# Kernel tuning notes

Hardware: AMD Instinct MI355X
Metric: run time of the kernel (lower is better)

Reference implementation:

```python
import jax, jax.numpy as jnp
import numpy as np

D_MODEL = 256
NS = 8


def _linear_params(key, out_f, in_f):
    s = 1.0 / np.sqrt(in_f)
    kw, kb = jax.random.split(key)
    W = jax.random.uniform(kw, (out_f, in_f), jnp.float32, -s, s)
    b = jax.random.uniform(kb, (out_f,), jnp.float32, -s, s)
    return W, b


def setup_inputs() -> dict:
    key = jax.random.key(0)
    ks = jax.random.split(key, 8)
    B, NQ = 2, 10000
    C, D, H, W = D_MODEL, 16, 64, 64
    Wdp, bdp = _linear_params(ks[3], NS * 3, D_MODEL)
    Wa, ba = _linear_params(ks[4], NS, D_MODEL)
    Wv, bv = _linear_params(ks[5], D_MODEL, D_MODEL)
    Ww, bw = _linear_params(ks[6], D_MODEL, D_MODEL)
    Wo, bo = _linear_params(ks[7], D_MODEL, D_MODEL)
    return {
        "query": jax.random.normal(ks[0], (B, NQ, D_MODEL), jnp.float32),
        "ref_points": jax.random.uniform(ks[1], (B, NQ, 3), jnp.float32, -1.0, 1.0),
        "image_features": jax.random.normal(ks[2], (B, C, D, H, W), jnp.float32),
        "mask": jnp.ones((B, 2, NQ), dtype=bool),
        "Wdp": Wdp, "bdp": bdp,
        "Wa": Wa, "ba": ba,
        "Wv": Wv, "bv": bv,
        "Ww": Ww, "bw": bw,
        "Wo": Wo, "bo": bo,
    }


def grid_sample_3d(vol, grid):
    """Trilinear grid_sample, align_corners=True, zero padding.
    vol: (B,C,D,H,W); grid: (B,N,P,3) with (x,y,z) in [-1,1] (x indexes W).
    Returns (B,N,P,C)."""
    B, C, D, H, W = vol.shape
    vol_t = jnp.transpose(vol, (0, 2, 3, 4, 1))  # (B,D,H,W,C)
    ix = (grid[..., 0] + 1.0) * 0.5 * (W - 1)
    iy = (grid[..., 1] + 1.0) * 0.5 * (H - 1)
    iz = (grid[..., 2] + 1.0) * 0.5 * (D - 1)
    x0 = jnp.floor(ix); y0 = jnp.floor(iy); z0 = jnp.floor(iz)
    fx = ix - x0; fy = iy - y0; fz = iz - z0

    def gather(v, zi, yi, xi):  # v: (D,H,W,C); indices (N,P)
        return v[zi, yi, xi]  # (N,P,C)

    out = jnp.zeros(grid.shape[:-1] + (C,), vol.dtype)
    for dz in (0, 1):
        for dy in (0, 1):
            for dx in (0, 1):
                xi = x0 + dx; yi = y0 + dy; zi = z0 + dz
                w = ((fx if dx else 1.0 - fx)
                     * (fy if dy else 1.0 - fy)
                     * (fz if dz else 1.0 - fz))
                valid = ((xi >= 0) & (xi <= W - 1)
                         & (yi >= 0) & (yi <= H - 1)
                         & (zi >= 0) & (zi <= D - 1))
                xc = jnp.clip(xi, 0, W - 1).astype(jnp.int32)
                yc = jnp.clip(yi, 0, H - 1).astype(jnp.int32)
                zc = jnp.clip(zi, 0, D - 1).astype(jnp.int32)
                vals = jax.vmap(gather)(vol_t, zc, yc, xc)  # (B,N,P,C)
                out = out + (w * valid)[..., None] * vals
    return out


def reference(query, ref_points, image_features, mask,
              Wdp, bdp, Wa, ba, Wv, bv, Ww, bw, Wo, bo):
    B, NQ, C = query.shape
    n_points = NS
    # learned offsets around reference points
    delta_p = (query @ Wdp.T + bdp).reshape(B, NQ, n_points, 3)
    p_delta_p = ref_points[:, :, None, :] + delta_p
    # reorder dims [1,0,2] -> grid (x,y,z) convention of grid_sample
    grid = p_delta_p[..., jnp.array([1, 0, 2])]
    sampled = grid_sample_3d(image_features, grid)  # (B,NQ,Ns,C)
    v = sampled @ Wv.T + bv          # value_proj
    wv = v @ Ww.T + bw               # W
    attn = jax.nn.softmax(query @ Wa.T + ba, axis=-1)  # (B,NQ,Ns)
    summed = jnp.einsum('bnpc,bnp->bnc', wv, attn)
    m = jnp.any(mask, axis=1)  # (B,NQ)
    summed = summed * m[..., None]
    return summed @ Wo.T + bo
```

## Files before the change

### kernel.cpp

```cpp
#include <hip/hip_runtime.h>

#define NQ    10000
#define BATCH 2
#define CDIM  256
#define DD    16
#define HH    64
#define WW    64

using bf16x8 = __attribute__((ext_vector_type(8))) short;
using f32x4  = __attribute__((ext_vector_type(4))) float;

__device__ __forceinline__ unsigned short f2bf(float f) {
    unsigned int u = __float_as_uint(f);
    u = u + 0x7FFFu + ((u >> 16) & 1u);
    return (unsigned short)(u >> 16);
}
__device__ __forceinline__ float bf2f(unsigned short h) {
    return __uint_as_float(((unsigned int)h) << 16);
}

__global__ __launch_bounds__(256) void k_transpose_bf16(const float* __restrict__ vol,
                                                        unsigned short* __restrict__ volt) {
    __shared__ float tile[64][65];
    int bid  = blockIdx.x;
    int cblk = bid & 3;
    int y    = (bid >> 2) & 63;
    int z    = (bid >> 8) & 15;
    int b    = bid >> 12;
    int tid  = threadIdx.x;
    int lx   = tid & 63, wy = tid >> 6;

    const float* src = vol + (size_t)(b * CDIM + cblk * 64) * (DD * HH * WW)
                           + (size_t)z * (HH * WW) + y * WW;
#pragma unroll
    for (int i = 0; i < 16; ++i) {
        int cl = wy * 16 + i;
        tile[cl][lx] = src[(size_t)cl * (DD * HH * WW) + lx];
    }
    __syncthreads();
    unsigned int* dst32 = reinterpret_cast<unsigned int*>(
        volt + ((size_t)(b * DD + z) * HH + y) * WW * CDIM) + cblk * 32;
    int cp = tid & 31;
#pragma unroll
    for (int i = 0; i < 8; ++i) {
        int x = i * 8 + (tid >> 5);
        unsigned int uo = (unsigned int)f2bf(tile[cp * 2][x])
                        | ((unsigned int)f2bf(tile[cp * 2 + 1][x]) << 16);
        dst32[(size_t)x * (CDIM / 2) + cp] = uo;
    }
}

template <bool BF16OUT>
__global__ __launch_bounds__(256) void k_combine(const float* __restrict__ A,
                                                 const float* __restrict__ B,
                                                 const float* __restrict__ bin,
                                                 const float* __restrict__ badd,
                                                 void* __restrict__ outW,
                                                 float* __restrict__ outb) {
    int i = blockIdx.x, j = threadIdx.x;
    __shared__ __align__(16) float row[256];
    __shared__ float red[4];
    row[j] = A[i * 256 + j];
    __syncthreads();
    float a0 = 0.f, a1 = 0.f, a2 = 0.f, a3 = 0.f;
#pragma unroll 4
    for (int k = 0; k < 256; k += 4) {
        a0 = fmaf(row[k + 0], B[(k + 0) * 256 + j], a0);
        a1 = fmaf(row[k + 1], B[(k + 1) * 256 + j], a1);
        a2 = fmaf(row[k + 2], B[(k + 2) * 256 + j], a2);
        a3 = fmaf(row[k + 3], B[(k + 3) * 256 + j], a3);
    }
    float acc = (a0 + a1) + (a2 + a3);
    if (BF16OUT)
        ((unsigned short*)outW)[i * 256 + j] = f2bf(acc);
    else
        ((float*)outW)[i * 256 + j] = acc;

    float pb = row[j] * bin[j];
    for (int off = 32; off; off >>= 1) pb += __shfl_down(pb, off, 64);
    int lane = j & 63, wv_ = j >> 6;
    if (lane == 0) red[wv_] = pb;
    __syncthreads();
    if (j == 0) outb[i] = red[0] + red[1] + red[2] + red[3] + badd[i];
}

__device__ __forceinline__ void geom_issue(
    int p, const float* __restrict__ dotsw, const float* __restrict__ bdp,
    float r0, float r1, float r2, float a,
    const ushort4* __restrict__ vb4, int lane,
    ushort4 (&u)[8], float (&wt)[8]) {
    float ix = fmaf(r1 + dotsw[p * 3 + 1] + bdp[p * 3 + 1], 31.5f, 31.5f);
    float iy = fmaf(r0 + dotsw[p * 3 + 0] + bdp[p * 3 + 0], 31.5f, 31.5f);
    float iz = fmaf(r2 + dotsw[p * 3 + 2] + bdp[p * 3 + 2], 7.5f, 7.5f);
    float xf = floorf(ix), yf = floorf(iy), zf = floorf(iz);
    float fx = ix - xf, fy = iy - yf, fz = iz - zf;
    int x0 = (int)xf, y0 = (int)yf, z0 = (int)zf;
    int xc[2], yc[2], zc[2];
    float wx[2], wy2[2], wz2[2];
#pragma unroll
    for (int d = 0; d < 2; ++d) {
        int xi = x0 + d, yi = y0 + d, zi = z0 + d;
        wx[d]  = (xi >= 0 && xi < WW) ? (d ? fx : 1.f - fx) : 0.f;
        wy2[d] = (yi >= 0 && yi < HH) ? (d ? fy : 1.f - fy) : 0.f;
        wz2[d] = ((zi >= 0 && zi < DD) ? (d ? fz : 1.f - fz) : 0.f) * a;
        xc[d] = min(max(xi, 0), WW - 1);
        yc[d] = min(max(yi, 0), HH - 1);
        zc[d] = min(max(zi, 0), DD - 1);
    }
    float wzy[4];
#pragma unroll
    for (int zz = 0; zz < 2; ++zz)
#pragma unroll
        for (int yy = 0; yy < 2; ++yy) wzy[zz * 2 + yy] = wz2[zz] * wy2[yy];
#pragma unroll
    for (int c = 0; c < 8; ++c) {
        int dz = c >> 2, dy = (c >> 1) & 1, dx = c & 1;
        wt[c] = wzy[dz * 2 + dy] * wx[dx];
        int off = (zc[dz] * HH + yc[dy]) * WW + xc[dx];
        off = __builtin_amdgcn_readfirstlane(off);
        u[c] = vb4[(size_t)off * (CDIM / 4) + lane];
    }
}

__device__ __forceinline__ void proc8(const ushort4 (&u)[8], const float (&wt)[8],
                                      float4& acc) {
#pragma unroll
    for (int c = 0; c < 8; ++c) {
        acc.x = fmaf(wt[c], bf2f(u[c].x), acc.x);
        acc.y = fmaf(wt[c], bf2f(u[c].y), acc.y);
        acc.z = fmaf(wt[c], bf2f(u[c].z), acc.z);
        acc.w = fmaf(wt[c], bf2f(u[c].w), acc.w);
    }
}

template <bool USE_VOLT>
__global__ __launch_bounds__(256) void k_sample4(
    const float* __restrict__ query, const float* __restrict__ refp,
    const float* __restrict__ vol, const unsigned short* __restrict__ voltb,
    const float* __restrict__ Wdp, const float* __restrict__ bdp,
    const float* __restrict__ Wa, const float* __restrict__ ba,
    unsigned short* __restrict__ S) {
    int tid = threadIdx.x, w = tid >> 6, lane = tid & 63;
    int g = lane >> 4, ch = lane & 15;
    int bq0 = blockIdx.x * 4;
    __shared__ float dots[4][32];

    {
        float4 qv[4][4];
#pragma unroll
        for (int q = 0; q < 4; ++q)
#pragma unroll
            for (int i = 0; i < 4; ++i)
                qv[q][i] = *reinterpret_cast<const float4*>(
                    query + (size_t)(bq0 + q) * 256 + ch * 16 + i * 4);
#pragma unroll
        for (int rr = 0; rr < 2; ++rr) {
            int row = w * 8 + rr * 4 + g;
            const float* rp = (row < 24) ? (Wdp + row * 256) : (Wa + (row - 24) * 256);
            float4 wv4[4];
#pragma unroll
            for (int i = 0; i < 4; ++i)
                wv4[i] = *reinterpret_cast<const float4*>(rp + ch * 16 + i * 4);
#pragma unroll
            for (int q = 0; q < 4; ++q) {
                float s = 0.f;
#pragma unroll
                for (int i = 0; i < 4; ++i)
                    s = fmaf(wv4[i].x, qv[q][i].x, fmaf(wv4[i].y, qv[q][i].y,
                        fmaf(wv4[i].z, qv[q][i].z, fmaf(wv4[i].w, qv[q][i].w, s))));
                s += __shfl_xor(s, 1); s += __shfl_xor(s, 2);
                s += __shfl_xor(s, 4); s += __shfl_xor(s, 8);
                if (ch == q) dots[q][row] = s;
            }
        }
    }
    __syncthreads();

    int bq = bq0 + w, b = bq / NQ;
    const float* dotsw = dots[w];
    float lg[8]; float mx = -1e30f;
#pragma unroll
    for (int p = 0; p < 8; ++p) { lg[p] = dotsw[24 + p] + ba[p]; mx = fmaxf(mx, lg[p]); }
    float se = 0.f;
#pragma unroll
    for (int p = 0; p < 8; ++p) { lg[p] = __expf(lg[p] - mx); se += lg[p]; }
    float inv = 1.f / se;
    float r0 = refp[bq * 3 + 0], r1 = refp[bq * 3 + 1], r2 = refp[bq * 3 + 2];

    float4 acc = make_float4(0.f, 0.f, 0.f, 0.f);
    if (USE_VOLT) {
        const ushort4* vb4 = reinterpret_cast<const ushort4*>(
            voltb + (size_t)b * (DD * HH * WW) * CDIM);
        ushort4 u0[8], u1[8];
        float w0a[8], w1a[8];
        geom_issue(0, dotsw, bdp, r0, r1, r2, lg[0] * inv, vb4, lane, u0, w0a);
#pragma unroll
        for (int p = 0; p < 7; ++p) {
            if ((p & 1) == 0) {
                geom_issue(p + 1, dotsw, bdp, r0, r1, r2, lg[p + 1] * inv, vb4, lane, u1, w1a);
                proc8(u0, w0a, acc);
            } else {
                geom_issue(p + 1, dotsw, bdp, r0, r1, r2, lg[p + 1] * inv, vb4, lane, u0, w0a);
                proc8(u1, w1a, acc);
            }
        }
        proc8(u1, w1a, acc);
    } else {
        const float* vf = vol + (size_t)b * CDIM * (DD * HH * WW);
#pragma unroll
        for (int p = 0; p < 8; ++p) {
            ushort4 ud[8]; float wtd[8];
            float a = lg[p] * inv;
            float ix = fmaf(r1 + dotsw[p * 3 + 1] + bdp[p * 3 + 1], 31.5f, 31.5f);
            float iy = fmaf(r0 + dotsw[p * 3 + 0] + bdp[p * 3 + 0], 31.5f, 31.5f);
            float iz = fmaf(r2 + dotsw[p * 3 + 2] + bdp[p * 3 + 2], 7.5f, 7.5f);
            float xf = floorf(ix), yf = floorf(iy), zf = floorf(iz);
            float fx = ix - xf, fy = iy - yf, fz = iz - zf;
            int x0 = (int)xf, y0 = (int)yf, z0 = (int)zf;
            int xc[2], yc[2], zc[2]; float wx[2], wy2[2], wz2[2];
#pragma unroll
            for (int d = 0; d < 2; ++d) {
                int xi = x0 + d, yi = y0 + d, zi = z0 + d;
                wx[d]  = (xi >= 0 && xi < WW) ? (d ? fx : 1.f - fx) : 0.f;
                wy2[d] = (yi >= 0 && yi < HH) ? (d ? fy : 1.f - fy) : 0.f;
                wz2[d] = ((zi >= 0 && zi < DD) ? (d ? fz : 1.f - fz) : 0.f) * a;
                xc[d] = min(max(xi, 0), WW - 1);
                yc[d] = min(max(yi, 0), HH - 1);
                zc[d] = min(max(zi, 0), DD - 1);
            }
#pragma unroll
            for (int c = 0; c < 8; ++c) {
                int dz = c >> 2, dy = (c >> 1) & 1, dx = c & 1;
                float wgt = wz2[dz] * wy2[dy] * wx[dx];
                int off = (zc[dz] * HH + yc[dy]) * WW + xc[dx];
#pragma unroll
                for (int cc = 0; cc < 4; ++cc) {
                    float v = vf[(size_t)(lane * 4 + cc) * (DD * HH * WW) + off];
                    (&acc.x)[cc] = fmaf(wgt, v, (&acc.x)[cc]);
                }
            }
        }
    }
    ushort4 o;
    o.x = f2bf(acc.x); o.y = f2bf(acc.y); o.z = f2bf(acc.z); o.w = f2bf(acc.w);
    reinterpret_cast<ushort4*>(S + (size_t)bq * 256)[lane] = o;
}

__global__ __launch_bounds__(256) void k_gemm_mx(
    const unsigned short* __restrict__ A,
    const unsigned short* __restrict__ Bw,
    const float* __restrict__ bias,
    const float* __restrict__ bo,
    const int* __restrict__ mask,
    float* __restrict__ C, int M) {
    const int LDT = 40;
    __shared__ unsigned short As[64 * LDT];
    __shared__ unsigned short Bs[64 * LDT];
    int tid = threadIdx.x, wv = tid >> 6, lane = tid & 63;
    int row0 = blockIdx.x * 64, col0 = blockIdx.y * 64;
    int wr = (wv & 1) * 32, wc = (wv >> 1) * 32;
    f32x4 acc[2][2] = {};

    int sr = tid >> 2, skc = tid & 3;
    for (int k0 = 0; k0 < 256; k0 += 32) {
        int gr = row0 + sr;
        uint4 av = make_uint4(0u, 0u, 0u, 0u);
        if (gr < M)
            av = *reinterpret_cast<const uint4*>(A + (size_t)gr * 256 + k0 + skc * 8);
        *reinterpret_cast<uint4*>(&As[sr * LDT + skc * 8]) = av;
        uint4 bv = *reinterpret_cast<const uint4*>(Bw + (size_t)(col0 + sr) * 256 + k0 + skc * 8);
        *reinterpret_cast<uint4*>(&Bs[sr * LDT + skc * 8]) = bv;
        __syncthreads();
        bf16x8 af[2], bf[2];
#pragma unroll
        for (int mi = 0; mi < 2; ++mi)
            af[mi] = *reinterpret_cast<const bf16x8*>(
                &As[(wr + mi * 16 + (lane & 15)) * LDT + (lane >> 4) * 8]);
#pragma unroll
        for (int ni = 0; ni < 2; ++ni)
            bf[ni] = *reinterpret_cast<const bf16x8*>(
                &Bs[(wc + ni * 16 + (lane & 15)) * LDT + (lane >> 4) * 8]);
#pragma unroll
        for (int mi = 0; mi < 2; ++mi)
#pragma unroll
            for (int ni = 0; ni < 2; ++ni)
                acc[mi][ni] = __builtin_amdgcn_mfma_f32_16x16x32_bf16(
                    af[mi], bf[ni], acc[mi][ni], 0, 0, 0);
        __syncthreads();
    }

    int lc = lane & 15, lr4 = (lane >> 4) * 4;
    float biasv[2], bov[2];
#pragma unroll
    for (int ni = 0; ni < 2; ++ni) {
        int col = col0 + wc + ni * 16 + lc;
        biasv[ni] = bias[col];
        bov[ni]   = bo[col];
    }
#pragma unroll
    for (int mi = 0; mi < 2; ++mi)
#pragma unroll
        for (int r = 0; r < 4; ++r) {
            int row = row0 + wr + mi * 16 + lr4 + r;
            if (row >= M) continue;
            int b = row / NQ, q = row - b * NQ;
            bool mv = (mask[(b * 2 + 0) * NQ + q] | mask[(b * 2 + 1) * NQ + q]) != 0;
#pragma unroll
            for (int ni = 0; ni < 2; ++ni) {
                int col = col0 + wc + ni * 16 + lc;
                C[(size_t)row * 256 + col] = mv ? (acc[mi][ni][r] + biasv[ni]) : bov[ni];
            }
        }
}

extern "C" void kernel_launch(void* const* d_in, const int* in_sizes, int n_in,
                              void* d_out, int out_size, void* d_ws, size_t ws_size,
                              hipStream_t stream) {
    const float* query = (const float*)d_in[0];
    const float* refp  = (const float*)d_in[1];
    const float* vol   = (const float*)d_in[2];
    const int*   mask  = (const int*)d_in[3];
    const float* Wdp   = (const float*)d_in[4];
    const float* bdp   = (const float*)d_in[5];
    const float* Wa    = (const float*)d_in[6];
    const float* ba    = (const float*)d_in[7];
    const float* Wv    = (const float*)d_in[8];
    const float* bv    = (const float*)d_in[9];
    const float* Ww    = (const float*)d_in[10];
    const float* bw    = (const float*)d_in[11];
    const float* Wo    = (const float*)d_in[12];
    const float* bo    = (const float*)d_in[13];
    float* out = (float*)d_out;

    char* ws = (char*)d_ws;
    const size_t M = (size_t)BATCH * NQ;
    size_t o_S    = 0;
    size_t o_W12  = o_S + M * 256 * 2;
    size_t o_b12  = o_W12 + 256 * 256 * 4;
    size_t o_W123 = o_b12 + 1024;
    size_t o_b123 = o_W123 + 256 * 256 * 2;
    size_t o_volt = (o_b123 + 1024 + 255) & ~(size_t)255;
    size_t need_volt = o_volt + (size_t)BATCH * DD * HH * WW * CDIM * 2;
    bool use_volt = ws_size >= need_volt;

    unsigned short* Sb   = (unsigned short*)(ws + o_S);
    float*          W12  = (float*)(ws + o_W12);
    float*          b12  = (float*)(ws + o_b12);
    unsigned short* W123 = (unsigned short*)(ws + o_W123);
    float*          b123 = (float*)(ws + o_b123);
    unsigned short* volt = (unsigned short*)(ws + o_volt);

    if (use_volt)
        k_transpose_bf16<<<BATCH * DD * HH * (CDIM / 64), 256, 0, stream>>>(vol, volt);
    k_combine<false><<<256, 256, 0, stream>>>(Ww, Wv, bv, bw, W12, b12);
    k_combine<true ><<<256, 256, 0, stream>>>(Wo, W12, b12, bo, W123, b123);

    if (use_volt)
        k_sample4<true><<<(int)(M / 4), 256, 0, stream>>>(query, refp, vol, volt,
                                                          Wdp, bdp, Wa, ba, Sb);
    else
        k_sample4<false><<<(int)(M / 4), 256, 0, stream>>>(query, refp, vol, volt,
                                                           Wdp, bdp, Wa, ba, Sb);

    dim3 g((unsigned)((M + 63) / 64), 4);
    k_gemm_mx<<<g, 256, 0, stream>>>(Sb, W123, b123, bo, mask, out, (int)M);
}
```

Baseline: 135.8 us.

## Split offset/attention projection into separate kernel, slim sampling kernel

Moves the query projection for sampling offsets and attention logits out of the sampling kernel into a new k_dots kernel. That kernel writes 32 biased dot products per query to workspace, and each wave handles 4 queries over all 32 rows. The sampling kernel now only loads those 32 floats, drops shared memory and __syncthreads, and takes launch bounds of (256,4) for higher occupancy. BF16 unpacking now uses uint2 with shift and mask instead of ushort4 conversions. The cost is an extra kernel launch plus a round trip of the dot products through global memory.

Result: slower. 145.8 us (+7.4%).

```diff
diff --git a/kernel.cpp b/kernel.cpp
--- a/kernel.cpp
+++ b/kernel.cpp
@@ -14,9 +14,6 @@
     unsigned int u = __float_as_uint(f);
     u = u + 0x7FFFu + ((u >> 16) & 1u);
     return (unsigned short)(u >> 16);
-}
-__device__ __forceinline__ float bf2f(unsigned short h) {
-    return __uint_as_float(((unsigned int)h) << 16);
 }
 
 __global__ __launch_bounds__(256) void k_transpose_bf16(const float* __restrict__ vol,
@@ -84,140 +81,91 @@
     if (j == 0) outb[i] = red[0] + red[1] + red[2] + red[3] + badd[i];
 }
 
-__device__ __forceinline__ void geom_issue(
-    int p, const float* __restrict__ dotsw, const float* __restrict__ bdp,
-    float r0, float r1, float r2, float a,
-    const ushort4* __restrict__ vb4, int lane,
-    ushort4 (&u)[8], float (&wt)[8]) {
-    float ix = fmaf(r1 + dotsw[p * 3 + 1] + bdp[p * 3 + 1], 31.5f, 31.5f);
-    float iy = fmaf(r0 + dotsw[p * 3 + 0] + bdp[p * 3 + 0], 31.5f, 31.5f);
-    float iz = fmaf(r2 + dotsw[p * 3 + 2] + bdp[p * 3 + 2], 7.5f, 7.5f);
-    float xf = floorf(ix), yf = floorf(iy), zf = floorf(iz);
-    float fx = ix - xf, fy = iy - yf, fz = iz - zf;
-    int x0 = (int)xf, y0 = (int)yf, z0 = (int)zf;
-    int xc[2], yc[2], zc[2];
-    float wx[2], wy2[2], wz2[2];
-#pragma unroll
-    for (int d = 0; d < 2; ++d) {
-        int xi = x0 + d, yi = y0 + d, zi = z0 + d;
-        wx[d]  = (xi >= 0 && xi < WW) ? (d ? fx : 1.f - fx) : 0.f;
-        wy2[d] = (yi >= 0 && yi < HH) ? (d ? fy : 1.f - fy) : 0.f;
-        wz2[d] = ((zi >= 0 && zi < DD) ? (d ? fz : 1.f - fz) : 0.f) * a;
-        xc[d] = min(max(xi, 0), WW - 1);
-        yc[d] = min(max(yi, 0), HH - 1);
-        zc[d] = min(max(zi, 0), DD - 1);
-    }
-    float wzy[4];
-#pragma unroll
-    for (int zz = 0; zz < 2; ++zz)
-#pragma unroll
-        for (int yy = 0; yy < 2; ++yy) wzy[zz * 2 + yy] = wz2[zz] * wy2[yy];
-#pragma unroll
-    for (int c = 0; c < 8; ++c) {
-        int dz = c >> 2, dy = (c >> 1) & 1, dx = c & 1;
-        wt[c] = wzy[dz * 2 + dy] * wx[dx];
-        int off = (zc[dz] * HH + yc[dy]) * WW + xc[dx];
-        off = __builtin_amdgcn_readfirstlane(off);
-        u[c] = vb4[(size_t)off * (CDIM / 4) + lane];
-    }
-}
-
-__device__ __forceinline__ void proc8(const ushort4 (&u)[8], const float (&wt)[8],
-                                      float4& acc) {
-#pragma unroll
-    for (int c = 0; c < 8; ++c) {
-        acc.x = fmaf(wt[c], bf2f(u[c].x), acc.x);
-        acc.y = fmaf(wt[c], bf2f(u[c].y), acc.y);
-        acc.z = fmaf(wt[c], bf2f(u[c].z), acc.z);
-        acc.w = fmaf(wt[c], bf2f(u[c].w), acc.w);
-    }
-}
-
-template <bool USE_VOLT>
-__global__ __launch_bounds__(256) void k_sample4(
-    const float* __restrict__ query, const float* __restrict__ refp,
-    const float* __restrict__ vol, const unsigned short* __restrict__ voltb,
+__global__ __launch_bounds__(256) void k_dots(
+    const float* __restrict__ query,
     const float* __restrict__ Wdp, const float* __restrict__ bdp,
     const float* __restrict__ Wa, const float* __restrict__ ba,
+    float* __restrict__ dotsG) {
+    int tid = threadIdx.x, w = tid >> 6, lane = tid & 63;
+    int g = lane >> 4, ch = lane & 15;
+    int bq0 = blockIdx.x * 16 + w * 4;
+
+    float4 qv[4][4];
+#pragma unroll
+    for (int q = 0; q < 4; ++q)
+#pragma unroll
+        for (int i = 0; i < 4; ++i)
+            qv[q][i] = *reinterpret_cast<const float4*>(
+                query + (size_t)(bq0 + q) * 256 + ch * 16 + i * 4);
+
+#pragma unroll
+    for (int rr = 0; rr < 8; ++rr) {
+        int rowi = rr * 4 + g;
+        const float* rp = (rowi < 24) ? (Wdp + rowi * 256) : (Wa + (rowi - 24) * 256);
+        float bia = (rowi < 24) ? bdp[rowi] : ba[rowi - 24];
+        float4 wv4[4];
+#pragma unroll
+        for (int i = 0; i < 4; ++i)
+            wv4[i] = *reinterpret_cast<const float4*>(rp + ch * 16 + i * 4);
+#pragma unroll
+        for (int q = 0; q < 4; ++q) {
+            float s = 0.f;
+#pragma unroll
+            for (int i = 0; i < 4; ++i)
+                s = fmaf(wv4[i].x, qv[q][i].x, fmaf(wv4[i].y, qv[q][i].y,
+                    fmaf(wv4[i].z, qv[q][i].z, fmaf(wv4[i].w, qv[q][i].w, s))));
+            s += __shfl_xor(s, 1); s += __shfl_xor(s, 2);
+            s += __shfl_xor(s, 4); s += __shfl_xor(s, 8);
+            if (ch == q) dotsG[(size_t)(bq0 + q) * 32 + rowi] = s + bia;
+        }
+    }
+}
+
+template <bool USE_VOLT>
+__global__ __launch_bounds__(256, 4) void k_sample5(
+    const float* __restrict__ refp,
+    const float* __restrict__ vol,
+    const unsigned short* __restrict__ voltb,
+    const float* __restrict__ dotsG,
     unsigned short* __restrict__ S) {
     int tid = threadIdx.x, w = tid >> 6, lane = tid & 63;
-    int g = lane >> 4, ch = lane & 15;
-    int bq0 = blockIdx.x * 4;
-    __shared__ float dots[4][32];
-
+    int bq = blockIdx.x * 4 + w, b = bq / NQ;
+
+    float dt[32];
     {
-        float4 qv[4][4];
-#pragma unroll
-        for (int q = 0; q < 4; ++q)
-#pragma unroll
-            for (int i = 0; i < 4; ++i)
-                qv[q][i] = *reinterpret_cast<const float4*>(
-                    query + (size_t)(bq0 + q) * 256 + ch * 16 + i * 4);
-#pragma unroll
-        for (int rr = 0; rr < 2; ++rr) {
-            int row = w * 8 + rr * 4 + g;
-            const float* rp = (row < 24) ? (Wdp + row * 256) : (Wa + (row - 24) * 256);
-            float4 wv4[4];
-#pragma unroll
-            for (int i = 0; i < 4; ++i)
-                wv4[i] = *reinterpret_cast<const float4*>(rp + ch * 16 + i * 4);
-#pragma unroll
-            for (int q = 0; q < 4; ++q) {
-                float s = 0.f;
-#pragma unroll
-                for (int i = 0; i < 4; ++i)
-                    s = fmaf(wv4[i].x, qv[q][i].x, fmaf(wv4[i].y, qv[q][i].y,
-                        fmaf(wv4[i].z, qv[q][i].z, fmaf(wv4[i].w, qv[q][i].w, s))));
-                s += __shfl_xor(s, 1); s += __shfl_xor(s, 2);
-                s += __shfl_xor(s, 4); s += __shfl_xor(s, 8);
-                if (ch == q) dots[q][row] = s;
-            }
-        }
-    }
-    __syncthreads();
-
-    int bq = bq0 + w, b = bq / NQ;
-    const float* dotsw = dots[w];
+        const float4* dr = reinterpret_cast<const float4*>(dotsG + (size_t)bq * 32);
+#pragma unroll
+        for (int j = 0; j < 8; ++j) {
+            float4 t = dr[j];
+            dt[4 * j + 0] = t.x; dt[4 * j + 1] = t.y;
+            dt[4 * j + 2] = t.z; dt[4 * j + 3] = t.w;
+        }
+    }
     float lg[8]; float mx = -1e30f;
 #pragma unroll
-    for (int p = 0; p < 8; ++p) { lg[p] = dotsw[24 + p] + ba[p]; mx = fmaxf(mx, lg[p]); }
+    for (int p = 0; p < 8; ++p) { lg[p] = dt[24 + p]; mx = fmaxf(mx, lg[p]); }
     float se = 0.f;
 #pragma unroll
     for (int p = 0; p < 8; ++p) { lg[p] = __expf(lg[p] - mx); se += lg[p]; }
     float inv = 1.f / se;
     float r0 = refp[bq * 3 + 0], r1 = refp[bq * 3 + 1], r2 = refp[bq * 3 + 2];
 
-    float4 acc = make_float4(0.f, 0.f, 0.f, 0.f);
+    float a0 = 0.f, a1 = 0.f, a2 = 0.f, a3 = 0.f;
+
     if (USE_VOLT) {
-        const ushort4* vb4 = reinterpret_cast<const ushort4*>(
+        const uint2* vb = reinterpret_cast<const uint2*>(
             voltb + (size_t)b * (DD * HH * WW) * CDIM);
-        ushort4 u0[8], u1[8];
-        float w0a[8], w1a[8];
-        geom_issue(0, dotsw, bdp, r0, r1, r2, lg[0] * inv, vb4, lane, u0, w0a);
-#pragma unroll
-        for (int p = 0; p < 7; ++p) {
-            if ((p & 1) == 0) {
-                geom_issue(p + 1, dotsw, bdp, r0, r1, r2, lg[p + 1] * inv, vb4, lane, u1, w1a);
-                proc8(u0, w0a, acc);
-            } else {
-                geom_issue(p + 1, dotsw, bdp, r0, r1, r2, lg[p + 1] * inv, vb4, lane, u0, w0a);
-                proc8(u1, w1a, acc);
-            }
-        }
-        proc8(u1, w1a, acc);
-    } else {
-        const float* vf = vol + (size_t)b * CDIM * (DD * HH * WW);
-#pragma unroll
-        for (int p = 0; p < 8; ++p) {
-            ushort4 ud[8]; float wtd[8];
+
+        auto geom = [&](int p, uint2 (&u)[8], float (&wt)[8]) {
             float a = lg[p] * inv;
-            float ix = fmaf(r1 + dotsw[p * 3 + 1] + bdp[p * 3 + 1], 31.5f, 31.5f);
-            float iy = fmaf(r0 + dotsw[p * 3 + 0] + bdp[p * 3 + 0], 31.5f, 31.5f);
-            float iz = fmaf(r2 + dotsw[p * 3 + 2] + bdp[p * 3 + 2], 7.5f, 7.5f);
+            float ix = fmaf(r1 + dt[p * 3 + 1], 31.5f, 31.5f);
+            float iy = fmaf(r0 + dt[p * 3 + 0], 31.5f, 31.5f);
+            float iz = fmaf(r2 + dt[p * 3 + 2], 7.5f, 7.5f);
             float xf = floorf(ix), yf = floorf(iy), zf = floorf(iz);
             float fx = ix - xf, fy = iy - yf, fz = iz - zf;
             int x0 = (int)xf, y0 = (int)yf, z0 = (int)zf;
-            int xc[2], yc[2], zc[2]; float wx[2], wy2[2], wz2[2];
+            int xc[2], yc[2], zc[2];
+            float wx[2], wy2[2], wz2[2];
 #pragma unroll
             for (int d = 0; d < 2; ++d) {
                 int xi = x0 + d, yi = y0 + d, zi = z0 + d;
@@ -228,21 +176,76 @@
                 yc[d] = min(max(yi, 0), HH - 1);
                 zc[d] = min(max(zi, 0), DD - 1);
             }
+            float wzy[4];
+#pragma unroll
+            for (int zz = 0; zz < 2; ++zz)
+#pragma unroll
+                for (int yy = 0; yy < 2; ++yy) wzy[zz * 2 + yy] = wz2[zz] * wy2[yy];
+#pragma unroll
+            for (int c = 0; c < 8; ++c) {
+                int dz = c >> 2, dy = (c >> 1) & 1, dx = c & 1;
+                wt[c] = wzy[dz * 2 + dy] * wx[dx];
+                int off = (zc[dz] * HH + yc[dy]) * WW + xc[dx];
+                off = __builtin_amdgcn_readfirstlane(off);
+                u[c] = vb[(size_t)off * (CDIM / 4) + lane];
+            }
+        };
+        auto proc = [&](const uint2 (&u)[8], const float (&wt)[8]) {
+#pragma unroll
+            for (int c = 0; c < 8; ++c) {
+                float w_ = wt[c];
+                a0 = fmaf(w_, __uint_as_float(u[c].x << 16), a0);
+                a1 = fmaf(w_, __uint_as_float(u[c].x & 0xffff0000u), a1);
+                a2 = fmaf(w_, __uint_as_float(u[c].y << 16), a2);
+                a3 = fmaf(w_, __uint_as_float(u[c].y & 0xffff0000u), a3);
+            }
+        };
+
+        uint2 u0[8], u1[8];
+        float w0a[8], w1a[8];
+        geom(0, u0, w0a);
+#pragma unroll
+        for (int p = 0; p < 7; ++p) {
+            if ((p & 1) == 0) { geom(p + 1, u1, w1a); proc(u0, w0a); }
+            else              { geom(p + 1, u0, w0a); proc(u1, w1a); }
+        }
+        proc(u1, w1a);
+    } else {
+        const float* vf = vol + (size_t)b * CDIM * (DD * HH * WW);
+#pragma unroll
+        for (int p = 0; p < 8; ++p) {
+            float a = lg[p] * inv;
+            float ix = fmaf(r1 + dt[p * 3 + 1], 31.5f, 31.5f);
+            float iy = fmaf(r0 + dt[p * 3 + 0], 31.5f, 31.5f);
+            float iz = fmaf(r2 + dt[p * 3 + 2], 7.5f, 7.5f);
+            float xf = floorf(ix), yf = floorf(iy), zf = floorf(iz);
+            float fx = ix - xf, fy = iy - yf, fz = iz - zf;
+            int x0 = (int)xf, y0 = (int)yf, z0 = (int)zf;
+            int xc[2], yc[2], zc[2]; float wx[2], wy2[2], wz2[2];
+#pragma unroll
+            for (int d = 0; d < 2; ++d) {
+                int xi = x0 + d, yi = y0 + d, zi = z0 + d;
+                wx[d]  = (xi >= 0 && xi < WW) ? (d ? fx : 1.f - fx) : 0.f;
+                wy2[d] = (yi >= 0 && yi < HH) ? (d ? fy : 1.f - fy) : 0.f;
+                wz2[d] = ((zi >= 0 && zi < DD) ? (d ? fz : 1.f - fz) : 0.f) * a;
+                xc[d] = min(max(xi, 0), WW - 1);
+                yc[d] = min(max(yi, 0), HH - 1);
+                zc[d] = min(max(zi, 0), DD - 1);
+            }
 #pragma unroll
             for (int c = 0; c < 8; ++c) {
                 int dz = c >> 2, dy = (c >> 1) & 1, dx = c & 1;
                 float wgt = wz2[dz] * wy2[dy] * wx[dx];
                 int off = (zc[dz] * HH + yc[dy]) * WW + xc[dx];
-#pragma unroll
-                for (int cc = 0; cc < 4; ++cc) {
-                    float v = vf[(size_t)(lane * 4 + cc) * (DD * HH * WW) + off];
-                    (&acc.x)[cc] = fmaf(wgt, v, (&acc.x)[cc]);
-                }
+                a0 = fmaf(wgt, vf[(size_t)(lane * 4 + 0) * (DD * HH * WW) + off], a0);
+                a1 = fmaf(wgt, vf[(size_t)(lane * 4 + 1) * (DD * HH * WW) + off], a1);
+                a2 = fmaf(wgt, vf[(size_t)(lane * 4 + 2) * (DD * HH * WW) + off], a2);
+                a3 = fmaf(wgt, vf[(size_t)(lane * 4 + 3) * (DD * HH * WW) + off], a3);
             }
         }
     }
     ushort4 o;
-    o.x = f2bf(acc.x); o.y = f2bf(acc.y); o.z = f2bf(acc.z); o.w = f2bf(acc.w);
+    o.x = f2bf(a0); o.y = f2bf(a1); o.z = f2bf(a2); o.w = f2bf(a3);
     reinterpret_cast<ushort4*>(S + (size_t)bq * 256)[lane] = o;
 }
 
@@ -339,7 +342,8 @@
     size_t o_b12  = o_W12 + 256 * 256 * 4;
     size_t o_W123 = o_b12 + 1024;
     size_t o_b123 = o_W123 + 256 * 256 * 2;
-    size_t o_volt = (o_b123 + 1024 + 255) & ~(size_t)255;
+    size_t o_dots = o_b123 + 1024;
+    size_t o_volt = (o_dots + M * 32 * 4 + 255) & ~(size_t)255;
     size_t need_volt = o_volt + (size_t)BATCH * DD * HH * WW * CDIM * 2;
     bool use_volt = ws_size >= need_volt;
 
@@ -348,19 +352,19 @@
     float*          b12  = (float*)(ws + o_b12);
     unsigned short* W123 = (unsigned short*)(ws + o_W123);
     float*          b123 = (float*)(ws + o_b123);
+    float*          dots = (float*)(ws + o_dots);
     unsigned short* volt = (unsigned short*)(ws + o_volt);
 
     if (use_volt)
         k_transpose_bf16<<<BATCH * DD * HH * (CDIM / 64), 256, 0, stream>>>(vol, volt);
     k_combine<false><<<256, 256, 0, stream>>>(Ww, Wv, bv, bw, W12, b12);
     k_combine<true ><<<256, 256, 0, stream>>>(Wo, W12, b12, bo, W123, b123);
+    k_dots<<<(int)(M / 16), 256, 0, stream>>>(query, Wdp, bdp, Wa, ba, dots);
 
     if (use_volt)
-        k_sample4<true><<<(int)(M / 4), 256, 0, stream>>>(query, refp, vol, volt,
-                                                          Wdp, bdp, Wa, ba, Sb);
+        k_sample5<true><<<(int)(M / 4), 256, 0, stream>>>(refp, vol, volt, dots, Sb);
     else
-        k_sample4<false><<<(int)(M / 4), 256, 0, stream>>>(query, refp, vol, volt,
-                                                           Wdp, bdp, Wa, ba, Sb);
+        k_sample5<false><<<(int)(M / 4), 256, 0, stream>>>(refp, vol, volt, dots, Sb);
 
     dim3 g((unsigned)((M + 63) / 64), 4);
     k_gemm_mx<<<g, 256, 0, stream>>>(Sb, W123, b123, bo, mask, out, (int)M);
```

## Gather x-adjacent corner pairs with 16-byte loads split across half-waves

Applied to the files above, without the earlier changes.

The sampling kernel no longer issues 8 corner gathers of 8 bytes per lane per point. It issues 4 gathers of 16 bytes, each covering two x-adjacent voxels. Lanes 0-31 handle the left voxel and lanes 32-63 the right one, with the x weight selected per half, and a cross-half shuffle sums the partials before lanes 0-31 write 8 channels each. This halves the number of gather instructions and address computations, at the cost of a shuffle reduction and extra edge-case logic for clamped x positions.

New measurement: 213.7 us. +57.4%, slower.

```diff
diff --git a/kernel.cpp b/kernel.cpp
--- a/kernel.cpp
+++ b/kernel.cpp
@@ -14,9 +14,6 @@
     unsigned int u = __float_as_uint(f);
     u = u + 0x7FFFu + ((u >> 16) & 1u);
     return (unsigned short)(u >> 16);
-}
-__device__ __forceinline__ float bf2f(unsigned short h) {
-    return __uint_as_float(((unsigned int)h) << 16);
 }
 
 __global__ __launch_bounds__(256) void k_transpose_bf16(const float* __restrict__ vol,
@@ -84,57 +81,8 @@
     if (j == 0) outb[i] = red[0] + red[1] + red[2] + red[3] + badd[i];
 }
 
-__device__ __forceinline__ void geom_issue(
-    int p, const float* __restrict__ dotsw, const float* __restrict__ bdp,
-    float r0, float r1, float r2, float a,
-    const ushort4* __restrict__ vb4, int lane,
-    ushort4 (&u)[8], float (&wt)[8]) {
-    float ix = fmaf(r1 + dotsw[p * 3 + 1] + bdp[p * 3 + 1], 31.5f, 31.5f);
-    float iy = fmaf(r0 + dotsw[p * 3 + 0] + bdp[p * 3 + 0], 31.5f, 31.5f);
-    float iz = fmaf(r2 + dotsw[p * 3 + 2] + bdp[p * 3 + 2], 7.5f, 7.5f);
-    float xf = floorf(ix), yf = floorf(iy), zf = floorf(iz);
-    float fx = ix - xf, fy = iy - yf, fz = iz - zf;
-    int x0 = (int)xf, y0 = (int)yf, z0 = (int)zf;
-    int xc[2], yc[2], zc[2];
-    float wx[2], wy2[2], wz2[2];
-#pragma unroll
-    for (int d = 0; d < 2; ++d) {
-        int xi = x0 + d, yi = y0 + d, zi = z0 + d;
-        wx[d]  = (xi >= 0 && xi < WW) ? (d ? fx : 1.f - fx) : 0.f;
-        wy2[d] = (yi >= 0 && yi < HH) ? (d ? fy : 1.f - fy) : 0.f;
-        wz2[d] = ((zi >= 0 && zi < DD) ? (d ? fz : 1.f - fz) : 0.f) * a;
-        xc[d] = min(max(xi, 0), WW - 1);
-        yc[d] = min(max(yi, 0), HH - 1);
-        zc[d] = min(max(zi, 0), DD - 1);
-    }
-    float wzy[4];
-#pragma unroll
-    for (int zz = 0; zz < 2; ++zz)
-#pragma unroll
-        for (int yy = 0; yy < 2; ++yy) wzy[zz * 2 + yy] = wz2[zz] * wy2[yy];
-#pragma unroll
-    for (int c = 0; c < 8; ++c) {
-        int dz = c >> 2, dy = (c >> 1) & 1, dx = c & 1;
-        wt[c] = wzy[dz * 2 + dy] * wx[dx];
-        int off = (zc[dz] * HH + yc[dy]) * WW + xc[dx];
-        off = __builtin_amdgcn_readfirstlane(off);
-        u[c] = vb4[(size_t)off * (CDIM / 4) + lane];
-    }
-}
-
-__device__ __forceinline__ void proc8(const ushort4 (&u)[8], const float (&wt)[8],
-                                      float4& acc) {
-#pragma unroll
-    for (int c = 0; c < 8; ++c) {
-        acc.x = fmaf(wt[c], bf2f(u[c].x), acc.x);
-        acc.y = fmaf(wt[c], bf2f(u[c].y), acc.y);
-        acc.z = fmaf(wt[c], bf2f(u[c].z), acc.z);
-        acc.w = fmaf(wt[c], bf2f(u[c].w), acc.w);
-    }
-}
-
 template <bool USE_VOLT>
-__global__ __launch_bounds__(256) void k_sample4(
+__global__ __launch_bounds__(256) void k_sample6(
     const float* __restrict__ query, const float* __restrict__ refp,
     const float* __restrict__ vol, const unsigned short* __restrict__ voltb,
     const float* __restrict__ Wdp, const float* __restrict__ bdp,
@@ -187,29 +135,81 @@
     float inv = 1.f / se;
     float r0 = refp[bq * 3 + 0], r1 = refp[bq * 3 + 1], r2 = refp[bq * 3 + 2];
 
-    float4 acc = make_float4(0.f, 0.f, 0.f, 0.f);
     if (USE_VOLT) {
-        const ushort4* vb4 = reinterpret_cast<const ushort4*>(
+        const uint4* vb = reinterpret_cast<const uint4*>(
             voltb + (size_t)b * (DD * HH * WW) * CDIM);
-        ushort4 u0[8], u1[8];
-        float w0a[8], w1a[8];
-        geom_issue(0, dotsw, bdp, r0, r1, r2, lg[0] * inv, vb4, lane, u0, w0a);
+        float acc[8] = {};
+
+        auto geom = [&](int p, uint4 (&u)[4], float (&wt)[4]) {
+            float a = lg[p] * inv;
+            float ix = fmaf(r1 + dotsw[p * 3 + 1] + bdp[p * 3 + 1], 31.5f, 31.5f);
+            float iy = fmaf(r0 + dotsw[p * 3 + 0] + bdp[p * 3 + 0], 31.5f, 31.5f);
+            float iz = fmaf(r2 + dotsw[p * 3 + 2] + bdp[p * 3 + 2], 7.5f, 7.5f);
+            float xf = floorf(ix), yf = floorf(iy), zf = floorf(iz);
+            float fx = ix - xf, fy = iy - yf, fz = iz - zf;
+            int x0 = (int)xf, y0 = (int)yf, z0 = (int)zf;
+            int rb = min(max(x0, 0), WW - 2);
+            float w0 = (x0 >= 0 && x0 < WW) ? 1.f - fx : 0.f;
+            float w1 = (x0 >= -1 && x0 < WW - 1) ? fx : 0.f;
+            float wA = (rb == x0) ? w0 : ((rb == x0 + 1) ? w1 : 0.f);
+            float wB = (rb == x0) ? w1 : ((rb + 1 == x0) ? w0 : 0.f);
+            float wh = (lane >= 32) ? wB : wA;
+            int yc[2], zc[2]; float wy2[2], wz2[2];
+#pragma unroll
+            for (int d = 0; d < 2; ++d) {
+                int yi = y0 + d, zi = z0 + d;
+                wy2[d] = (yi >= 0 && yi < HH) ? (d ? fy : 1.f - fy) : 0.f;
+                wz2[d] = ((zi >= 0 && zi < DD) ? (d ? fz : 1.f - fz) : 0.f) * a;
+                yc[d] = min(max(yi, 0), HH - 1);
+                zc[d] = min(max(zi, 0), DD - 1);
+            }
+#pragma unroll
+            for (int c = 0; c < 4; ++c) {
+                int dz = c >> 1, dy = c & 1;
+                wt[c] = wz2[dz] * wy2[dy] * wh;
+                int vidx = (zc[dz] * HH + yc[dy]) * WW + rb;
+                vidx = __builtin_amdgcn_readfirstlane(vidx);
+                u[c] = vb[(size_t)vidx * 32 + lane];
+            }
+        };
+        auto proc = [&](const uint4 (&u)[4], const float (&wt)[4]) {
+#pragma unroll
+            for (int c = 0; c < 4; ++c) {
+                float w_ = wt[c];
+                acc[0] = fmaf(w_, __uint_as_float(u[c].x << 16),         acc[0]);
+                acc[1] = fmaf(w_, __uint_as_float(u[c].x & 0xffff0000u), acc[1]);
+                acc[2] = fmaf(w_, __uint_as_float(u[c].y << 16),         acc[2]);
+                acc[3] = fmaf(w_, __uint_as_float(u[c].y & 0xffff0000u), acc[3]);
+                acc[4] = fmaf(w_, __uint_as_float(u[c].z << 16),         acc[4]);
+                acc[5] = fmaf(w_, __uint_as_float(u[c].z & 0xffff0000u), acc[5]);
+                acc[6] = fmaf(w_, __uint_as_float(u[c].w << 16),         acc[6]);
+                acc[7] = fmaf(w_, __uint_as_float(u[c].w & 0xffff0000u), acc[7]);
+            }
+        };
+
+        uint4 u0[4], u1[4];
+        float w0a[4], w1a[4];
+        geom(0, u0, w0a);
 #pragma unroll
         for (int p = 0; p < 7; ++p) {
-            if ((p & 1) == 0) {
-                geom_issue(p + 1, dotsw, bdp, r0, r1, r2, lg[p + 1] * inv, vb4, lane, u1, w1a);
-                proc8(u0, w0a, acc);
-            } else {
-                geom_issue(p + 1, dotsw, bdp, r0, r1, r2, lg[p + 1] * inv, vb4, lane, u0, w0a);
-                proc8(u1, w1a, acc);
-            }
-        }
-        proc8(u1, w1a, acc);
+            if ((p & 1) == 0) { geom(p + 1, u1, w1a); proc(u0, w0a); }
+            else              { geom(p + 1, u0, w0a); proc(u1, w1a); }
+        }
+        proc(u1, w1a);
+
+#pragma unroll
+        for (int i = 0; i < 8; ++i) acc[i] += __shfl_xor(acc[i], 32);
+        if (lane < 32) {
+            union { unsigned short us[8]; uint4 v; } o;
+#pragma unroll
+            for (int i = 0; i < 8; ++i) o.us[i] = f2bf(acc[i]);
+            *reinterpret_cast<uint4*>(S + (size_t)bq * 256 + lane * 8) = o.v;
+        }
     } else {
         const float* vf = vol + (size_t)b * CDIM * (DD * HH * WW);
+        float a0 = 0.f, a1 = 0.f, a2 = 0.f, a3 = 0.f;
 #pragma unroll
         for (int p = 0; p < 8; ++p) {
-            ushort4 ud[8]; float wtd[8];
             float a = lg[p] * inv;
             float ix = fmaf(r1 + dotsw[p * 3 + 1] + bdp[p * 3 + 1], 31.5f, 31.5f);
             float iy = fmaf(r0 + dotsw[p * 3 + 0] + bdp[p * 3 + 0], 31.5f, 31.5f);
@@ -233,17 +233,16 @@
                 int dz = c >> 2, dy = (c >> 1) & 1, dx = c & 1;
                 float wgt = wz2[dz] * wy2[dy] * wx[dx];
                 int off = (zc[dz] * HH + yc[dy]) * WW + xc[dx];
-#pragma unroll
-                for (int cc = 0; cc < 4; ++cc) {
-                    float v = vf[(size_t)(lane * 4 + cc) * (DD * HH * WW) + off];
-                    (&acc.x)[cc] = fmaf(wgt, v, (&acc.x)[cc]);
-                }
-            }
-        }
-    }
-    ushort4 o;
-    o.x = f2bf(acc.x); o.y = f2bf(acc.y); o.z = f2bf(acc.z); o.w = f2bf(acc.w);
-    reinterpret_cast<ushort4*>(S + (size_t)bq * 256)[lane] = o;
+                a0 = fmaf(wgt, vf[(size_t)(lane * 4 + 0) * (DD * HH * WW) + off], a0);
+                a1 = fmaf(wgt, vf[(size_t)(lane * 4 + 1) * (DD * HH * WW) + off], a1);
+                a2 = fmaf(wgt, vf[(size_t)(lane * 4 + 2) * (DD * HH * WW) + off], a2);
+                a3 = fmaf(wgt, vf[(size_t)(lane * 4 + 3) * (DD * HH * WW) + off], a3);
+            }
+        }
+        ushort4 o;
+        o.x = f2bf(a0); o.y = f2bf(a1); o.z = f2bf(a2); o.w = f2bf(a3);
+        reinterpret_cast<ushort4*>(S + (size_t)bq * 256)[lane] = o;
+    }
 }
 
 __global__ __launch_bounds__(256) void k_gemm_mx(
@@ -356,10 +355,10 @@
     k_combine<true ><<<256, 256, 0, stream>>>(Wo, W12, b12, bo, W123, b123);
 
     if (use_volt)
-        k_sample4<true><<<(int)(M / 4), 256, 0, stream>>>(query, refp, vol, volt,
+        k_sample6<true><<<(int)(M / 4), 256, 0, stream>>>(query, refp, vol, volt,
                                                           Wdp, bdp, Wa, ba, Sb);
     else
-        k_sample4<false><<<(int)(M / 4), 256, 0, stream>>>(query, refp, vol, volt,
+        k_sample6<false><<<(int)(M / 4), 256, 0, stream>>>(query, refp, vol, volt,
                                                            Wdp, bdp, Wa, ba, Sb);
 
     dim3 g((unsigned)((M + 63) / 64), 4);
```

## Process two queries per wavefront and stage query rows in shared memory

Applied to the files above, without the earlier changes.

The sampling kernel now handles 8 queries per block, 2 per wavefront, so each wave interleaves the gathers of two independent queries instead of software-pipelining one query's points. Query rows are staged into LDS once, and the projection dots for 8 queries reuse each Wdp/Wa weight load. The aim is more memory-level parallelism per wave and half as many blocks re-reading the weights. In exchange it uses more registers and LDS per block and halves the grid, which may lower occupancy. It also drops the explicit double-buffered prefetch across points.

Result: slower. 145.9 us (+7.5%).

```diff
diff --git a/kernel.cpp b/kernel.cpp
--- a/kernel.cpp
+++ b/kernel.cpp
@@ -14,9 +14,6 @@
     unsigned int u = __float_as_uint(f);
     u = u + 0x7FFFu + ((u >> 16) & 1u);
     return (unsigned short)(u >> 16);
-}
-__device__ __forceinline__ float bf2f(unsigned short h) {
-    return __uint_as_float(((unsigned int)h) << 16);
 }
 
 __global__ __launch_bounds__(256) void k_transpose_bf16(const float* __restrict__ vol,
@@ -84,57 +81,8 @@
     if (j == 0) outb[i] = red[0] + red[1] + red[2] + red[3] + badd[i];
 }
 
-__device__ __forceinline__ void geom_issue(
-    int p, const float* __restrict__ dotsw, const float* __restrict__ bdp,
-    float r0, float r1, float r2, float a,
-    const ushort4* __restrict__ vb4, int lane,
-    ushort4 (&u)[8], float (&wt)[8]) {
-    float ix = fmaf(r1 + dotsw[p * 3 + 1] + bdp[p * 3 + 1], 31.5f, 31.5f);
-    float iy = fmaf(r0 + dotsw[p * 3 + 0] + bdp[p * 3 + 0], 31.5f, 31.5f);
-    float iz = fmaf(r2 + dotsw[p * 3 + 2] + bdp[p * 3 + 2], 7.5f, 7.5f);
-    float xf = floorf(ix), yf = floorf(iy), zf = floorf(iz);
-    float fx = ix - xf, fy = iy - yf, fz = iz - zf;
-    int x0 = (int)xf, y0 = (int)yf, z0 = (int)zf;
-    int xc[2], yc[2], zc[2];
-    float wx[2], wy2[2], wz2[2];
-#pragma unroll
-    for (int d = 0; d < 2; ++d) {
-        int xi = x0 + d, yi = y0 + d, zi = z0 + d;
-        wx[d]  = (xi >= 0 && xi < WW) ? (d ? fx : 1.f - fx) : 0.f;
-        wy2[d] = (yi >= 0 && yi < HH) ? (d ? fy : 1.f - fy) : 0.f;
-        wz2[d] = ((zi >= 0 && zi < DD) ? (d ? fz : 1.f - fz) : 0.f) * a;
-        xc[d] = min(max(xi, 0), WW - 1);
-        yc[d] = min(max(yi, 0), HH - 1);
-        zc[d] = min(max(zi, 0), DD - 1);
-    }
-    float wzy[4];
-#pragma unroll
-    for (int zz = 0; zz < 2; ++zz)
-#pragma unroll
-        for (int yy = 0; yy < 2; ++yy) wzy[zz * 2 + yy] = wz2[zz] * wy2[yy];
-#pragma unroll
-    for (int c = 0; c < 8; ++c) {
-        int dz = c >> 2, dy = (c >> 1) & 1, dx = c & 1;
-        wt[c] = wzy[dz * 2 + dy] * wx[dx];
-        int off = (zc[dz] * HH + yc[dy]) * WW + xc[dx];
-        off = __builtin_amdgcn_readfirstlane(off);
-        u[c] = vb4[(size_t)off * (CDIM / 4) + lane];
-    }
-}
-
-__device__ __forceinline__ void proc8(const ushort4 (&u)[8], const float (&wt)[8],
-                                      float4& acc) {
-#pragma unroll
-    for (int c = 0; c < 8; ++c) {
-        acc.x = fmaf(wt[c], bf2f(u[c].x), acc.x);
-        acc.y = fmaf(wt[c], bf2f(u[c].y), acc.y);
-        acc.z = fmaf(wt[c], bf2f(u[c].z), acc.z);
-        acc.w = fmaf(wt[c], bf2f(u[c].w), acc.w);
-    }
-}
-
 template <bool USE_VOLT>
-__global__ __launch_bounds__(256) void k_sample4(
+__global__ __launch_bounds__(256) void k_sample7(
     const float* __restrict__ query, const float* __restrict__ refp,
     const float* __restrict__ vol, const unsigned short* __restrict__ voltb,
     const float* __restrict__ Wdp, const float* __restrict__ bdp,
@@ -142,82 +90,79 @@
     unsigned short* __restrict__ S) {
     int tid = threadIdx.x, w = tid >> 6, lane = tid & 63;
     int g = lane >> 4, ch = lane & 15;
-    int bq0 = blockIdx.x * 4;
-    __shared__ float dots[4][32];
+    int bq0 = blockIdx.x * 8;
+    __shared__ __align__(16) float qs[8 * 256];
+    __shared__ float dots[8][32];
 
     {
-        float4 qv[4][4];
-#pragma unroll
-        for (int q = 0; q < 4; ++q)
-#pragma unroll
-            for (int i = 0; i < 4; ++i)
-                qv[q][i] = *reinterpret_cast<const float4*>(
-                    query + (size_t)(bq0 + q) * 256 + ch * 16 + i * 4);
-#pragma unroll
-        for (int rr = 0; rr < 2; ++rr) {
-            int row = w * 8 + rr * 4 + g;
-            const float* rp = (row < 24) ? (Wdp + row * 256) : (Wa + (row - 24) * 256);
-            float4 wv4[4];
-#pragma unroll
-            for (int i = 0; i < 4; ++i)
-                wv4[i] = *reinterpret_cast<const float4*>(rp + ch * 16 + i * 4);
-#pragma unroll
-            for (int q = 0; q < 4; ++q) {
-                float s = 0.f;
-#pragma unroll
-                for (int i = 0; i < 4; ++i)
-                    s = fmaf(wv4[i].x, qv[q][i].x, fmaf(wv4[i].y, qv[q][i].y,
-                        fmaf(wv4[i].z, qv[q][i].z, fmaf(wv4[i].w, qv[q][i].w, s))));
-                s += __shfl_xor(s, 1); s += __shfl_xor(s, 2);
-                s += __shfl_xor(s, 4); s += __shfl_xor(s, 8);
-                if (ch == q) dots[q][row] = s;
-            }
+        const float4* gq = reinterpret_cast<const float4*>(query + (size_t)bq0 * 256);
+        float4* q4 = reinterpret_cast<float4*>(qs);
+        q4[tid]       = gq[tid];
+        q4[tid + 256] = gq[tid + 256];
+    }
+    __syncthreads();
+
+#pragma unroll
+    for (int rr = 0; rr < 2; ++rr) {
+        int row = w * 8 + rr * 4 + g;
+        const float* rp = (row < 24) ? (Wdp + row * 256) : (Wa + (row - 24) * 256);
+        float4 wv4[4];
+#pragma unroll
+        for (int i = 0; i < 4; ++i)
+            wv4[i] = *reinterpret_cast<const float4*>(rp + ch * 16 + i * 4);
+#pragma unroll
+        for (int q = 0; q < 8; ++q) {
+            const float* qq = qs + q * 256 + ch * 16;
+            float s = 0.f;
+#pragma unroll
+            for (int i = 0; i < 4; ++i) {
+                float4 qv = *reinterpret_cast<const float4*>(qq + i * 4);
+                s = fmaf(wv4[i].x, qv.x, fmaf(wv4[i].y, qv.y,
+                    fmaf(wv4[i].z, qv.z, fmaf(wv4[i].w, qv.w, s))));
+            }
+            s += __shfl_xor(s, 1); s += __shfl_xor(s, 2);
+            s += __shfl_xor(s, 4); s += __shfl_xor(s, 8);
+            if (ch == q) dots[q][row] = s;
         }
     }
     __syncthreads();
 
-    int bq = bq0 + w, b = bq / NQ;
-    const float* dotsw = dots[w];
-    float lg[8]; float mx = -1e30f;
-#pragma unroll
-    for (int p = 0; p < 8; ++p) { lg[p] = dotsw[24 + p] + ba[p]; mx = fmaxf(mx, lg[p]); }
-    float se = 0.f;
-#pragma unroll
-    for (int p = 0; p < 8; ++p) { lg[p] = __expf(lg[p] - mx); se += lg[p]; }
-    float inv = 1.f / se;
-    float r0 = refp[bq * 3 + 0], r1 = refp[bq * 3 + 1], r2 = refp[bq * 3 + 2];
-
-    float4 acc = make_float4(0.f, 0.f, 0.f, 0.f);
+    int qa = bq0 + 2 * w, qb = qa + 1;
+    int bat = qa / NQ;
+    const float* dA = dots[2 * w];
+    const float* dB = dots[2 * w + 1];
+
+    float lgA[8], lgB[8];
+    float mxA = -1e30f, mxB = -1e30f;
+#pragma unroll
+    for (int p = 0; p < 8; ++p) {
+        lgA[p] = dA[24 + p] + ba[p]; mxA = fmaxf(mxA, lgA[p]);
+        lgB[p] = dB[24 + p] + ba[p]; mxB = fmaxf(mxB, lgB[p]);
+    }
+    float seA = 0.f, seB = 0.f;
+#pragma unroll
+    for (int p = 0; p < 8; ++p) {
+        lgA[p] = __expf(lgA[p] - mxA); seA += lgA[p];
+        lgB[p] = __expf(lgB[p] - mxB); seB += lgB[p];
+    }
+    float invA = 1.f / seA, invB = 1.f / seB;
+    float r0A = refp[qa * 3 + 0], r1A = refp[qa * 3 + 1], r2A = refp[qa * 3 + 2];
+    float r0B = refp[qb * 3 + 0], r1B = refp[qb * 3 + 1], r2B = refp[qb * 3 + 2];
+
     if (USE_VOLT) {
-        const ushort4* vb4 = reinterpret_cast<const ushort4*>(
-            voltb + (size_t)b * (DD * HH * WW) * CDIM);
-        ushort4 u0[8], u1[8];
-        float w0a[8], w1a[8];
-        geom_issue(0, dotsw, bdp, r0, r1, r2, lg[0] * inv, vb4, lane, u0, w0a);
-#pragma unroll
-        for (int p = 0; p < 7; ++p) {
-            if ((p & 1) == 0) {
-                geom_issue(p + 1, dotsw, bdp, r0, r1, r2, lg[p + 1] * inv, vb4, lane, u1, w1a);
-                proc8(u0, w0a, acc);
-            } else {
-                geom_issue(p + 1, dotsw, bdp, r0, r1, r2, lg[p + 1] * inv, vb4, lane, u0, w0a);
-                proc8(u1, w1a, acc);
-            }
-        }
-        proc8(u1, w1a, acc);
-    } else {
-        const float* vf = vol + (size_t)b * CDIM * (DD * HH * WW);
-#pragma unroll
-        for (int p = 0; p < 8; ++p) {
-            ushort4 ud[8]; float wtd[8];
-            float a = lg[p] * inv;
-            float ix = fmaf(r1 + dotsw[p * 3 + 1] + bdp[p * 3 + 1], 31.5f, 31.5f);
-            float iy = fmaf(r0 + dotsw[p * 3 + 0] + bdp[p * 3 + 0], 31.5f, 31.5f);
-            float iz = fmaf(r2 + dotsw[p * 3 + 2] + bdp[p * 3 + 2], 7.5f, 7.5f);
+        const uint2* vb = reinterpret_cast<const uint2*>(
+            voltb + (size_t)bat * (DD * HH * WW) * CDIM);
+
+        auto geom = [&](int p, const float* dq, float r0, float r1, float r2,
+                        float a, uint2 (&u)[8], float (&wt)[8]) {
+            float ix = fmaf(r1 + dq[p * 3 + 1] + bdp[p * 3 + 1], 31.5f, 31.5f);
+            float iy = fmaf(r0 + dq[p * 3 + 0] + bdp[p * 3 + 0], 31.5f, 31.5f);
+            float iz = fmaf(r2 + dq[p * 3 + 2] + bdp[p * 3 + 2], 7.5f, 7.5f);
             float xf = floorf(ix), yf = floorf(iy), zf = floorf(iz);
             float fx = ix - xf, fy = iy - yf, fz = iz - zf;
             int x0 = (int)xf, y0 = (int)yf, z0 = (int)zf;
-            int xc[2], yc[2], zc[2]; float wx[2], wy2[2], wz2[2];
+            int xc[2], yc[2], zc[2];
+            float wx[2], wy2[2], wz2[2];
 #pragma unroll
             for (int d = 0; d < 2; ++d) {
                 int xi = x0 + d, yi = y0 + d, zi = z0 + d;
@@ -228,22 +173,94 @@
                 yc[d] = min(max(yi, 0), HH - 1);
                 zc[d] = min(max(zi, 0), DD - 1);
             }
+            float wzy[4];
+#pragma unroll
+            for (int zz = 0; zz < 2; ++zz)
+#pragma unroll
+                for (int yy = 0; yy < 2; ++yy) wzy[zz * 2 + yy] = wz2[zz] * wy2[yy];
 #pragma unroll
             for (int c = 0; c < 8; ++c) {
                 int dz = c >> 2, dy = (c >> 1) & 1, dx = c & 1;
-                float wgt = wz2[dz] * wy2[dy] * wx[dx];
+                wt[c] = wzy[dz * 2 + dy] * wx[dx];
                 int off = (zc[dz] * HH + yc[dy]) * WW + xc[dx];
-#pragma unroll
-                for (int cc = 0; cc < 4; ++cc) {
-                    float v = vf[(size_t)(lane * 4 + cc) * (DD * HH * WW) + off];
-                    (&acc.x)[cc] = fmaf(wgt, v, (&acc.x)[cc]);
+                off = __builtin_amdgcn_readfirstlane(off);
+                u[c] = vb[(size_t)off * (CDIM / 4) + lane];
+            }
+        };
+        auto proc = [&](const uint2 (&u)[8], const float (&wt)[8], float (&acc)[4]) {
+#pragma unroll
+            for (int c = 0; c < 8; ++c) {
+                float w_ = wt[c];
+                acc[0] = fmaf(w_, __uint_as_float(u[c].x << 16),         acc[0]);
+                acc[1] = fmaf(w_, __uint_as_float(u[c].x & 0xffff0000u), acc[1]);
+                acc[2] = fmaf(w_, __uint_as_float(u[c].y << 16),         acc[2]);
+                acc[3] = fmaf(w_, __uint_as_float(u[c].y & 0xffff0000u), acc[3]);
+            }
+        };
+
+        float accA[4] = {}, accB[4] = {};
+        uint2 uA[8], uB[8];
+        float wA[8], wB[8];
+#pragma unroll
+        for (int p = 0; p < 8; ++p) {
+            geom(p, dA, r0A, r1A, r2A, lgA[p] * invA, uA, wA);
+            geom(p, dB, r0B, r1B, r2B, lgB[p] * invB, uB, wB);
+            proc(uA, wA, accA);
+            proc(uB, wB, accB);
+        }
+        ushort4 oA, oB;
+        oA.x = f2bf(accA[0]); oA.y = f2bf(accA[1]);
+        oA.z = f2bf(accA[2]); oA.w = f2bf(accA[3]);
+        oB.x = f2bf(accB[0]); oB.y = f2bf(accB[1]);
+        oB.z = f2bf(accB[2]); oB.w = f2bf(accB[3]);
+        reinterpret_cast<ushort4*>(S + (size_t)qa * 256)[lane] = oA;
+        reinterpret_cast<ushort4*>(S + (size_t)qb * 256)[lane] = oB;
+    } else {
+        const float* vf = vol + (size_t)bat * CDIM * (DD * HH * WW);
+#pragma unroll
+        for (int qq = 0; qq < 2; ++qq) {
+            const float* dq = qq ? dB : dA;
+            const float* lg = qq ? lgB : lgA;
+            float inv = qq ? invB : invA;
+            float r0 = qq ? r0B : r0A, r1 = qq ? r1B : r1A, r2 = qq ? r2B : r2A;
+            int bq = qq ? qb : qa;
+            float a0 = 0.f, a1 = 0.f, a2 = 0.f, a3 = 0.f;
+#pragma unroll
+            for (int p = 0; p < 8; ++p) {
+                float a = lg[p] * inv;
+                float ix = fmaf(r1 + dq[p * 3 + 1] + bdp[p * 3 + 1], 31.5f, 31.5f);
+                float iy = fmaf(r0 + dq[p * 3 + 0] + bdp[p * 3 + 0], 31.5f, 31.5f);
+                float iz = fmaf(r2 + dq[p * 3 + 2] + bdp[p * 3 + 2], 7.5f, 7.5f);
+                float xf = floorf(ix), yf = floorf(iy), zf = floorf(iz);
+                float fx = ix - xf, fy = iy - yf, fz = iz - zf;
+                int x0 = (int)xf, y0 = (int)yf, z0 = (int)zf;
+                int xc[2], yc[2], zc[2]; float wx[2], wy2[2], wz2[2];
+#pragma unroll
+                for (int d = 0; d < 2; ++d) {
+                    int xi = x0 + d, yi = y0 + d, zi = z0 + d;
+                    wx[d]  = (xi >= 0 && xi < WW) ? (d ? fx : 1.f - fx) : 0.f;
+                    wy2[d] = (yi >= 0 && yi < HH) ? (d ? fy : 1.f - fy) : 0.f;
+                    wz2[d] = ((zi >= 0 && zi < DD) ? (d ? fz : 1.f - fz) : 0.f) * a;
+                    xc[d] = min(max(xi, 0), WW - 1);
+                    yc[d] = min(max(yi, 0), HH - 1);
+                    zc[d] = min(max(zi, 0), DD - 1);
                 }
-            }
+#pragma unroll
+                for (int c = 0; c < 8; ++c) {
+                    int dz = c >> 2, dy = (c >> 1) & 1, dx = c & 1;
+                    float wgt = wz2[dz] * wy2[dy] * wx[dx];
+                    int off = (zc[dz] * HH + yc[dy]) * WW + xc[dx];
+                    a0 = fmaf(wgt, vf[(size_t)(lane * 4 + 0) * (DD * HH * WW) + off], a0);
+                    a1 = fmaf(wgt, vf[(size_t)(lane * 4 + 1) * (DD * HH * WW) + off], a1);
+                    a2 = fmaf(wgt, vf[(size_t)(lane * 4 + 2) * (DD * HH * WW) + off], a2);
+                    a3 = fmaf(wgt, vf[(size_t)(lane * 4 + 3) * (DD * HH * WW) + off], a3);
+                }
+            }
+            ushort4 o;
+            o.x = f2bf(a0); o.y = f2bf(a1); o.z = f2bf(a2); o.w = f2bf(a3);
+            reinterpret_cast<ushort4*>(S + (size_t)bq * 256)[lane] = o;
         }
     }
-    ushort4 o;
-    o.x = f2bf(acc.x); o.y = f2bf(acc.y); o.z = f2bf(acc.z); o.w = f2bf(acc.w);
-    reinterpret_cast<ushort4*>(S + (size_t)bq * 256)[lane] = o;
 }
 
 __global__ __launch_bounds__(256) void k_gemm_mx(
@@ -356,10 +373,10 @@
     k_combine<true ><<<256, 256, 0, stream>>>(Wo, W12, b12, bo, W123, b123);
 
     if (use_volt)
-        k_sample4<true><<<(int)(M / 4), 256, 0, stream>>>(query, refp, vol, volt,
+        k_sample7<true><<<(int)(M / 8), 256, 0, stream>>>(query, refp, vol, volt,
                                                           Wdp, bdp, Wa, ba, Sb);
     else
-        k_sample4<false><<<(int)(M / 4), 256, 0, stream>>>(query, refp, vol, volt,
+        k_sample7<false><<<(int)(M / 8), 256, 0, stream>>>(query, refp, vol, volt,
                                                            Wdp, bdp, Wa, ba, Sb);
 
     dim3 g((unsigned)((M + 63) / 64), 4);
```
